# Kernel tuning notes

Hardware: AMD Instinct MI355X
Metric: run time of the kernel (lower is better)

Reference implementation:

```python
import jax, jax.numpy as jnp
import numpy as np

GROUP_SIZE = 64

def _dequant_w4(qweight, wscales):
    """Unpack int4 weights and apply per-(group, out-channel) scales.
    qweight: [N, K//2] uint8-valued ints, low nibble = even k, high nibble = odd k.
    wscales: [K//GROUP_SIZE, N] float. Returns [N, K] float weight.
    """
    q = qweight.astype(jnp.int32)
    low = (q & 15) - 8          # [N, K//2], signed int4
    high = ((q >> 4) & 15) - 8  # [N, K//2]
    N = q.shape[0]
    K = q.shape[1] * 2
    w_int = jnp.stack([low, high], axis=-1).reshape(N, K)  # interleaved low/high
    # scale[n, k] = wscales[k // GROUP_SIZE, n]
    scale = jnp.repeat(wscales, GROUP_SIZE, axis=0).T  # [N, K]
    return w_int.astype(wscales.dtype) * scale

def setup_inputs() -> dict:
    key = jax.random.key(0)
    ks = jax.random.split(key, 7)
    M, K, N, R = 8192, 4096, 4096, 32
    x = jax.random.normal(ks[0], (M, K), dtype=jnp.float32)
    qweight = jax.random.randint(ks[1], (N, K // 2), 0, 256, dtype=jnp.int32)
    wscales = jax.random.uniform(ks[2], (K // GROUP_SIZE, N), dtype=jnp.float32) * 0.01 + 0.001
    proj_down = jax.random.normal(ks[3], (R, K), dtype=jnp.float32) * 0.02
    proj_up = jax.random.normal(ks[4], (N, R), dtype=jnp.float32) * 0.02
    wtscale = jnp.ones((1,), dtype=jnp.float32)
    bias = jax.random.normal(ks[5], (N,), dtype=jnp.float32) * 0.01
    return {"x": x, "qweight": qweight, "wscales": wscales,
            "proj_down": proj_down, "proj_up": proj_up,
            "wtscale": wtscale, "bias": bias}

def reference(x, qweight, wscales, proj_down, proj_up, wtscale, bias):
    # Dequant int4 weight, GEMM, low-rank LoRA correction scaled by wtscale, bias.
    w = _dequant_w4(qweight, wscales)              # [N, K]
    out = x @ w.T                                  # [M, N]
    lora = (x @ proj_down.T) @ proj_up.T           # [M, R] @ [R, N] -> [M, N]
    out = out + lora * wtscale
    out = out + bias
    return out
```

## Files before the change

### kernel.cpp

```cpp
#include <hip/hip_runtime.h>
#include <hip/hip_bf16.h>
#include <stdint.h>

#define MD 8192
#define ND 4096
#define KD 4096
#define RD 32

typedef __bf16 bf16x8 __attribute__((ext_vector_type(8)));
typedef float f32x4 __attribute__((ext_vector_type(4)));

__device__ __forceinline__ void cp16(const void* g, void* l) {
    __builtin_amdgcn_global_load_lds(
        (const __attribute__((address_space(1))) void*)g,
        (__attribute__((address_space(3))) void*)l, 16, 0, 0);
}

__global__ __launch_bounds__(256) void cvt_x(const float* __restrict__ x,
                                             __hip_bfloat16* __restrict__ y) {
    size_t i = ((size_t)blockIdx.x * 256 + threadIdx.x) * 8;
    float4 a = *(const float4*)(x + i);
    float4 b = *(const float4*)(x + i + 4);
    union { __hip_bfloat16 h[8]; uint4 u; } o;
    o.h[0] = __float2bfloat16(a.x); o.h[1] = __float2bfloat16(a.y);
    o.h[2] = __float2bfloat16(a.z); o.h[3] = __float2bfloat16(a.w);
    o.h[4] = __float2bfloat16(b.x); o.h[5] = __float2bfloat16(b.y);
    o.h[6] = __float2bfloat16(b.z); o.h[7] = __float2bfloat16(b.w);
    *(uint4*)(y + i) = o.u;
}

__global__ __launch_bounds__(256) void build_weff(
    const int* __restrict__ qw,
    const float* __restrict__ wsc,
    const float* __restrict__ pd,
    const float* __restrict__ pu,
    const float* __restrict__ wts_p,
    __hip_bfloat16* __restrict__ weff)
{
    __shared__ float pd_s[RD][132];
    __shared__ float pu_t[RD][68];
    const int t = threadIdx.x;
    const int kb = blockIdx.x * 128;
    const int nb = blockIdx.y * 64;

    for (int f = t; f < (RD * 128) / 4; f += 256) {
        int r = f >> 5;
        int c = (f & 31) << 2;
        *(float4*)&pd_s[r][c] = *(const float4*)(pd + (size_t)r * KD + kb + c);
    }
    for (int f = t; f < (64 * RD) / 4; f += 256) {
        int nl = f >> 3;
        int r4 = (f & 7) << 2;
        float4 v = *(const float4*)(pu + (size_t)(nb + nl) * RD + r4);
        pu_t[r4 + 0][nl] = v.x; pu_t[r4 + 1][nl] = v.y;
        pu_t[r4 + 2][nl] = v.z; pu_t[r4 + 3][nl] = v.w;
    }
    __syncthreads();

    const float wts = wts_p[0];
    const int kc = (t & 15) << 3;
    const int ng = (t >> 4) << 2;

    float acc[4][8];
#pragma unroll
    for (int i = 0; i < 4; ++i)
#pragma unroll
        for (int j = 0; j < 8; ++j) acc[i][j] = 0.f;

    for (int r = 0; r < RD; ++r) {
        float4 pda = *(const float4*)&pd_s[r][kc];
        float4 pdb = *(const float4*)&pd_s[r][kc + 4];
        float4 puv = *(const float4*)&pu_t[r][ng];
        float pus[4] = {puv.x, puv.y, puv.z, puv.w};
        float pdv[8] = {pda.x, pda.y, pda.z, pda.w, pdb.x, pdb.y, pdb.z, pdb.w};
#pragma unroll
        for (int i = 0; i < 4; ++i)
#pragma unroll
            for (int j = 0; j < 8; ++j)
                acc[i][j] += pus[i] * pdv[j];
    }

    const int kg = kb + kc;
    const int g = kg >> 6;
#pragma unroll
    for (int i = 0; i < 4; ++i) {
        const int n = nb + ng + i;
        const float sc = wsc[(size_t)g * ND + n];
        int4 q = *(const int4*)(qw + (size_t)n * (KD / 2) + (kg >> 1));
        const int qi[4] = {q.x, q.y, q.z, q.w};
        union { __hip_bfloat16 h[8]; uint4 u; } o;
#pragma unroll
        for (int j = 0; j < 4; ++j) {
            const int lo = (qi[j] & 15) - 8;
            const int hi = ((qi[j] >> 4) & 15) - 8;
            o.h[2 * j]     = __float2bfloat16((float)lo * sc + wts * acc[i][2 * j]);
            o.h[2 * j + 1] = __float2bfloat16((float)hi * sc + wts * acc[i][2 * j + 1]);
        }
        *(uint4*)(weff + (size_t)n * KD + kg) = o.u;
    }
}

#define FENCE asm volatile("" ::: "memory")
#define VMW4 asm volatile("s_waitcnt vmcnt(4)" ::: "memory")
#define VMW2 asm volatile("s_waitcnt vmcnt(2)" ::: "memory")
#define VMW0 asm volatile("s_waitcnt vmcnt(0)" ::: "memory")
#define VMNONE
#define ENDB __builtin_amdgcn_s_barrier(); FENCE
#define ENDNONE

#define PHASE(QI, QJ, CB, STAGE, WAITM, ENDM)                                  \
    {                                                                          \
        bf16x8 af[4][2], bfr[2][2];                                            \
        const char* Ab = ArowBase + (CB) + (QI) * 8192;                        \
        const char* Bb = BrowBase + (CB) + (QJ) * 4096;                        \
        _Pragma("unroll") for (int i = 0; i < 4; ++i) {                        \
            af[i][0] = *(const bf16x8*)(Ab + i * 2048 + slh0);                 \
            af[i][1] = *(const bf16x8*)(Ab + i * 2048 + slh1);                 \
        }                                                                      \
        _Pragma("unroll") for (int j = 0; j < 2; ++j) {                        \
            bfr[j][0] = *(const bf16x8*)(Bb + j * 2048 + slh0);                \
            bfr[j][1] = *(const bf16x8*)(Bb + j * 2048 + slh1);               \
        }                                                                      \
        STAGE;                                                                 \
        WAITM;                                                                 \
        __builtin_amdgcn_s_barrier();                                          \
        asm volatile("s_waitcnt lgkmcnt(0)" ::: "memory");                     \
        __builtin_amdgcn_sched_barrier(0);                                     \
        __builtin_amdgcn_s_setprio(1);                                         \
        _Pragma("unroll") for (int i = 0; i < 4; ++i)                          \
            _Pragma("unroll") for (int j = 0; j < 2; ++j) {                    \
                acc[(QI) * 4 + i][(QJ) * 2 + j] =                              \
                    __builtin_amdgcn_mfma_f32_16x16x32_bf16(                   \
                        af[i][0], bfr[j][0], acc[(QI) * 4 + i][(QJ) * 2 + j],  \
                        0, 0, 0);                                              \
                acc[(QI) * 4 + i][(QJ) * 2 + j] =                              \
                    __builtin_amdgcn_mfma_f32_16x16x32_bf16(                   \
                        af[i][1], bfr[j][1], acc[(QI) * 4 + i][(QJ) * 2 + j],  \
                        0, 0, 0);                                              \
            }                                                                  \
        __builtin_amdgcn_s_setprio(0);                                         \
        ENDM;                                                                  \
    }

__global__ __launch_bounds__(512, 2) void gemm_bt_bias(
    const __hip_bfloat16* __restrict__ A,
    const __hip_bfloat16* __restrict__ B,
    const float* __restrict__ bias,
    float* __restrict__ C)
{
    __shared__ alignas(16) char As[2][32768];
    __shared__ alignas(16) char Bs[2][32768];

    const int t = threadIdx.x;
    const int lane = t & 63;
    const int w = t >> 6;
    const int wm = w >> 2;
    const int wn = w & 3;

    const int bid = blockIdx.x;
    const int swz = (bid & 7) * 64 + (bid >> 3);
    const int m0 = (swz >> 4) * 256;
    const int n0 = (swz & 15) * 256;

    const int lrow = lane >> 3;
    const int gch = (lane & 7) ^ lrow;
    const __hip_bfloat16* Ag = A + (size_t)(m0 + lrow) * KD + gch * 8;
    const __hip_bfloat16* Bg = B + (size_t)(n0 + lrow) * KD + gch * 8;

    const int a1 = w, a2 = 16 + w, a3 = 8 + w, a4 = 24 + w;
    const int bq = wm * 8 + wn;
    const int b1 = bq, b2 = bq + 16, b3 = bq + 4, b4 = bq + 20;

    const int qm = lane & 15;
    const int c4 = lane >> 4;
    const int slh0 = (c4 ^ (qm & 7)) * 16;
    const int slh1 = ((4 + c4) ^ (qm & 7)) * 16;
    const char* ArowBase = (const char*)As + (wm * 128 + qm) * 128;
    const char* BrowBase = (const char*)Bs + (wn * 64 + qm) * 128;

    cp16(Ag + (size_t)a1 * 8 * KD, (char*)As + a1 * 1024);
    cp16(Ag + (size_t)a2 * 8 * KD, (char*)As + a2 * 1024);
    cp16(Bg + (size_t)b1 * 8 * KD, (char*)Bs + b1 * 1024);
    cp16(Bg + (size_t)b2 * 8 * KD, (char*)Bs + b2 * 1024);
    cp16(Ag + (size_t)a3 * 8 * KD, (char*)As + a3 * 1024);
    cp16(Ag + (size_t)a4 * 8 * KD, (char*)As + a4 * 1024);
    cp16(Bg + (size_t)b3 * 8 * KD, (char*)Bs + b3 * 1024);
    cp16(Bg + (size_t)b4 * 8 * KD, (char*)Bs + b4 * 1024);

    f32x4 acc[8][4];
#pragma unroll
    for (int i = 0; i < 8; ++i)
#pragma unroll
        for (int j = 0; j < 4; ++j) acc[i][j] = (f32x4){0.f, 0.f, 0.f, 0.f};

    VMW4;
    __builtin_amdgcn_s_barrier();
    FENCE;

    for (int kt = 0; kt < 63; ++kt) {
        const int cb = (kt & 1) << 15;
        const int sb = cb ^ 32768;
        const size_t ko = (size_t)(kt + 1) * 64;
        PHASE(0, 0, cb,
              (cp16(Ag + (size_t)a1 * 8 * KD + ko, (char*)As + sb + a1 * 1024),
               cp16(Ag + (size_t)a2 * 8 * KD + ko, (char*)As + sb + a2 * 1024)),
              VMW4, ENDB)
        PHASE(1, 0, cb,
              (cp16(Bg + (size_t)b1 * 8 * KD + ko, (char*)Bs + sb + b1 * 1024),
               cp16(Bg + (size_t)b2 * 8 * KD + ko, (char*)Bs + sb + b2 * 1024)),
              VMW4, ENDB)
        PHASE(0, 1, cb,
              (cp16(Ag + (size_t)a3 * 8 * KD + ko, (char*)As + sb + a3 * 1024),
               cp16(Ag + (size_t)a4 * 8 * KD + ko, (char*)As + sb + a4 * 1024)),
              VMNONE, ENDB)
        PHASE(1, 1, cb,
              (cp16(Bg + (size_t)b3 * 8 * KD + ko, (char*)Bs + sb + b3 * 1024),
               cp16(Bg + (size_t)b4 * 8 * KD + ko, (char*)Bs + sb + b4 * 1024)),
              VMW4, ENDB)
    }
    PHASE(0, 0, 32768, ((void)0), VMW2, ENDB)
    PHASE(1, 0, 32768, ((void)0), VMW0, ENDB)
    PHASE(0, 1, 32768, ((void)0), VMNONE, ENDB)
    PHASE(1, 1, 32768, ((void)0), VMNONE, ENDNONE)

    const int cm = (lane >> 4) << 2;
    const int cn = lane & 15;
#pragma unroll
    for (int j = 0; j < 4; ++j) {
        const int n = n0 + wn * 64 + j * 16 + cn;
        const float bv = bias[n];
#pragma unroll
        for (int i = 0; i < 8; ++i) {
            float* dst = C + (size_t)(m0 + wm * 128 + i * 16 + cm) * ND + n;
#pragma unroll
            for (int r = 0; r < 4; ++r)
                dst[(size_t)r * ND] = acc[i][j][r] + bv;
        }
    }
}

extern "C" void kernel_launch(void* const* d_in, const int* in_sizes, int n_in,
                              void* d_out, int out_size, void* d_ws, size_t ws_size,
                              hipStream_t stream) {
    const float* x    = (const float*)d_in[0];
    const int* qw     = (const int*)d_in[1];
    const float* wsc  = (const float*)d_in[2];
    const float* pd   = (const float*)d_in[3];
    const float* pu   = (const float*)d_in[4];
    const float* wts  = (const float*)d_in[5];
    const float* bias = (const float*)d_in[6];
    float* out = (float*)d_out;

    __hip_bfloat16* weff = (__hip_bfloat16*)d_ws;
    __hip_bfloat16* xbf  = (__hip_bfloat16*)((char*)d_ws + (size_t)ND * KD * sizeof(__hip_bfloat16));

    cvt_x<<<(MD * (size_t)KD) / (256 * 8), 256, 0, stream>>>(x, xbf);
    build_weff<<<dim3(KD / 128, ND / 64), 256, 0, stream>>>(qw, wsc, pd, pu, wts, weff);
    gemm_bt_bias<<<512, 512, 0, stream>>>(xbf, weff, bias, out);
}
```

Baseline: 588.4 us.

## Restructure GEMM main loop into two K-half phases with one barrier per tile

```diff
diff --git a/kernel.cpp b/kernel.cpp
--- a/kernel.cpp
+++ b/kernel.cpp
@@ -101,45 +101,22 @@
 }
 
 #define FENCE asm volatile("" ::: "memory")
-#define VMW4 asm volatile("s_waitcnt vmcnt(4)" ::: "memory")
-#define VMW2 asm volatile("s_waitcnt vmcnt(2)" ::: "memory")
-#define VMW0 asm volatile("s_waitcnt vmcnt(0)" ::: "memory")
-#define VMNONE
-#define ENDB __builtin_amdgcn_s_barrier(); FENCE
-#define ENDNONE
-
-#define PHASE(QI, QJ, CB, STAGE, WAITM, ENDM)                                  \
+
+#define PHASEH(CB, SL)                                                         \
     {                                                                          \
-        bf16x8 af[4][2], bfr[2][2];                                            \
-        const char* Ab = ArowBase + (CB) + (QI) * 8192;                        \
-        const char* Bb = BrowBase + (CB) + (QJ) * 4096;                        \
-        _Pragma("unroll") for (int i = 0; i < 4; ++i) {                        \
-            af[i][0] = *(const bf16x8*)(Ab + i * 2048 + slh0);                 \
-            af[i][1] = *(const bf16x8*)(Ab + i * 2048 + slh1);                 \
-        }                                                                      \
-        _Pragma("unroll") for (int j = 0; j < 2; ++j) {                        \
-            bfr[j][0] = *(const bf16x8*)(Bb + j * 2048 + slh0);                \
-            bfr[j][1] = *(const bf16x8*)(Bb + j * 2048 + slh1);               \
-        }                                                                      \
-        STAGE;                                                                 \
-        WAITM;                                                                 \
-        __builtin_amdgcn_s_barrier();                                          \
+        bf16x8 af[8], bf[4];                                                   \
+        _Pragma("unroll") for (int i = 0; i < 8; ++i)                          \
+            af[i] = *(const bf16x8*)(ArowB + (CB) + i * 2048 + (SL));          \
+        _Pragma("unroll") for (int j = 0; j < 4; ++j)                          \
+            bf[j] = *(const bf16x8*)(BrowB + (CB) + j * 2048 + (SL));          \
         asm volatile("s_waitcnt lgkmcnt(0)" ::: "memory");                     \
         __builtin_amdgcn_sched_barrier(0);                                     \
         __builtin_amdgcn_s_setprio(1);                                         \
-        _Pragma("unroll") for (int i = 0; i < 4; ++i)                          \
-            _Pragma("unroll") for (int j = 0; j < 2; ++j) {                    \
-                acc[(QI) * 4 + i][(QJ) * 2 + j] =                              \
-                    __builtin_amdgcn_mfma_f32_16x16x32_bf16(                   \
-                        af[i][0], bfr[j][0], acc[(QI) * 4 + i][(QJ) * 2 + j],  \
-                        0, 0, 0);                                              \
-                acc[(QI) * 4 + i][(QJ) * 2 + j] =                              \
-                    __builtin_amdgcn_mfma_f32_16x16x32_bf16(                   \
-                        af[i][1], bfr[j][1], acc[(QI) * 4 + i][(QJ) * 2 + j],  \
-                        0, 0, 0);                                              \
-            }                                                                  \
+        _Pragma("unroll") for (int i = 0; i < 8; ++i)                          \
+            _Pragma("unroll") for (int j = 0; j < 4; ++j)                      \
+                acc[i][j] = __builtin_amdgcn_mfma_f32_16x16x32_bf16(           \
+                    af[i], bf[j], acc[i][j], 0, 0, 0);                         \
         __builtin_amdgcn_s_setprio(0);                                         \
-        ENDM;                                                                  \
     }
 
 __global__ __launch_bounds__(512, 2) void gemm_bt_bias(
@@ -167,25 +144,12 @@
     const __hip_bfloat16* Ag = A + (size_t)(m0 + lrow) * KD + gch * 8;
     const __hip_bfloat16* Bg = B + (size_t)(n0 + lrow) * KD + gch * 8;
 
-    const int a1 = w, a2 = 16 + w, a3 = 8 + w, a4 = 24 + w;
-    const int bq = wm * 8 + wn;
-    const int b1 = bq, b2 = bq + 16, b3 = bq + 4, b4 = bq + 20;
-
     const int qm = lane & 15;
     const int c4 = lane >> 4;
     const int slh0 = (c4 ^ (qm & 7)) * 16;
     const int slh1 = ((4 + c4) ^ (qm & 7)) * 16;
-    const char* ArowBase = (const char*)As + (wm * 128 + qm) * 128;
-    const char* BrowBase = (const char*)Bs + (wn * 64 + qm) * 128;
-
-    cp16(Ag + (size_t)a1 * 8 * KD, (char*)As + a1 * 1024);
-    cp16(Ag + (size_t)a2 * 8 * KD, (char*)As + a2 * 1024);
-    cp16(Bg + (size_t)b1 * 8 * KD, (char*)Bs + b1 * 1024);
-    cp16(Bg + (size_t)b2 * 8 * KD, (char*)Bs + b2 * 1024);
-    cp16(Ag + (size_t)a3 * 8 * KD, (char*)As + a3 * 1024);
-    cp16(Ag + (size_t)a4 * 8 * KD, (char*)As + a4 * 1024);
-    cp16(Bg + (size_t)b3 * 8 * KD, (char*)Bs + b3 * 1024);
-    cp16(Bg + (size_t)b4 * 8 * KD, (char*)Bs + b4 * 1024);
+    const char* ArowB = (const char*)As + (wm * 128 + qm) * 128;
+    const char* BrowB = (const char*)Bs + (wn * 64 + qm) * 128;
 
     f32x4 acc[8][4];
 #pragma unroll
@@ -193,7 +157,13 @@
 #pragma unroll
         for (int j = 0; j < 4; ++j) acc[i][j] = (f32x4){0.f, 0.f, 0.f, 0.f};
 
-    VMW4;
+#pragma unroll
+    for (int q = 0; q < 4; ++q) {
+        const int blk = w + 8 * q;
+        cp16(Ag + (size_t)blk * 8 * KD, (char*)As + blk * 1024);
+        cp16(Bg + (size_t)blk * 8 * KD, (char*)Bs + blk * 1024);
+    }
+    asm volatile("s_waitcnt vmcnt(0)" ::: "memory");
     __builtin_amdgcn_s_barrier();
     FENCE;
 
@@ -201,27 +171,20 @@
         const int cb = (kt & 1) << 15;
         const int sb = cb ^ 32768;
         const size_t ko = (size_t)(kt + 1) * 64;
-        PHASE(0, 0, cb,
-              (cp16(Ag + (size_t)a1 * 8 * KD + ko, (char*)As + sb + a1 * 1024),
-               cp16(Ag + (size_t)a2 * 8 * KD + ko, (char*)As + sb + a2 * 1024)),
-              VMW4, ENDB)
-        PHASE(1, 0, cb,
-              (cp16(Bg + (size_t)b1 * 8 * KD + ko, (char*)Bs + sb + b1 * 1024),
-               cp16(Bg + (size_t)b2 * 8 * KD + ko, (char*)Bs + sb + b2 * 1024)),
-              VMW4, ENDB)
-        PHASE(0, 1, cb,
-              (cp16(Ag + (size_t)a3 * 8 * KD + ko, (char*)As + sb + a3 * 1024),
-               cp16(Ag + (size_t)a4 * 8 * KD + ko, (char*)As + sb + a4 * 1024)),
-              VMNONE, ENDB)
-        PHASE(1, 1, cb,
-              (cp16(Bg + (size_t)b3 * 8 * KD + ko, (char*)Bs + sb + b3 * 1024),
-               cp16(Bg + (size_t)b4 * 8 * KD + ko, (char*)Bs + sb + b4 * 1024)),
-              VMW4, ENDB)
-    }
-    PHASE(0, 0, 32768, ((void)0), VMW2, ENDB)
-    PHASE(1, 0, 32768, ((void)0), VMW0, ENDB)
-    PHASE(0, 1, 32768, ((void)0), VMNONE, ENDB)
-    PHASE(1, 1, 32768, ((void)0), VMNONE, ENDNONE)
+#pragma unroll
+        for (int q = 0; q < 4; ++q) {
+            const int blk = w + 8 * q;
+            cp16(Ag + (size_t)blk * 8 * KD + ko, (char*)As + sb + blk * 1024);
+            cp16(Bg + (size_t)blk * 8 * KD + ko, (char*)Bs + sb + blk * 1024);
+        }
+        PHASEH(cb, slh0)
+        PHASEH(cb, slh1)
+        asm volatile("s_waitcnt vmcnt(0)" ::: "memory");
+        __builtin_amdgcn_s_barrier();
+        FENCE;
+    }
+    PHASEH(32768, slh0)
+    PHASEH(32768, slh1)
 
     const int cm = (lane >> 4) << 2;
     const int cn = lane & 15;
```

New measurement: 553.7 us. 5.9% less time.
